# Kernel tuning notes

Measured on AMD Instinct MI355X. Metric: run time of the kernel, lower is better.

The kernel has to match this reference:

```python
import jax, jax.numpy as jnp
import numpy as np

B, CIN, COUT, H, W = 16, 128, 128, 64, 64
E, PS, FF = 8, 16, 8
GC, HID, HC = 4 * FF, 64, COUT * 4  # gate_channel, gate hidden, bottleneck hidden


def conv(x, w, stride=1, pad=0, groups=1):
    # x: [B,C,H,W], w: [O,I/groups,kh,kw]
    return jax.lax.conv_general_dilated(
        x, w, (stride, stride), [(pad, pad), (pad, pad)], feature_group_count=groups)


def group_norm(x, scale, bias, groups, eps=1e-5):
    b, c = x.shape[:2]
    xr = x.reshape(b, groups, c // groups, *x.shape[2:])
    m = xr.mean(axis=(2, 3, 4), keepdims=True)
    v = xr.var(axis=(2, 3, 4), keepdims=True)
    xr = (xr - m) * jax.lax.rsqrt(v + eps)
    return xr.reshape(x.shape) * scale[None, :, None, None] + bias[None, :, None, None]


def setup_inputs() -> dict:
    key = jax.random.key(0)
    ks = jax.random.split(key, 8)
    f = lambda k, shp: jax.random.normal(k, shp, jnp.float32) * 0.05
    return dict(
        x=jax.random.normal(ks[0], (B, CIN, H, W), jnp.float32),
        w_exp=f(ks[1], (E, COUT, CIN, 3, 3)),
        gn_exp_s=jnp.ones((E, COUT), jnp.float32),
        gn_exp_b=jnp.zeros((E, COUT), jnp.float32),
        w1=f(ks[2], (GC, HID)), b1=jnp.zeros((HID,), jnp.float32),
        w2=f(ks[3], (HID, E)), b2=jnp.zeros((E,), jnp.float32),
        w_pw1=f(ks[4], (HC, COUT, 1, 1)),
        gn1_s=jnp.ones((HC,), jnp.float32), gn1_b=jnp.zeros((HC,), jnp.float32),
        w_dw=f(ks[5], (HC, 1, 3, 3)),
        gn2_s=jnp.ones((HC,), jnp.float32), gn2_b=jnp.zeros((HC,), jnp.float32),
        w_pw2=f(ks[6], (COUT, HC, 1, 1)),
        gn3_s=jnp.ones((COUT,), jnp.float32), gn3_b=jnp.zeros((COUT,), jnp.float32),
    )


def reference(x, w_exp, gn_exp_s, gn_exp_b, w1, b1, w2, b2,
              w_pw1, gn1_s, gn1_b, w_dw, gn2_s, gn2_b, w_pw2, gn3_s, gn3_b):
    # ---- Conv experts (residual 3x3 conv + GN + SiLU), vmapped over experts ----
    def expert(w, s, b):
        y = conv(x, w, pad=1)
        y = group_norm(y, s, b, groups=min(8, COUT))
        return jax.nn.silu(y) + x  # use_residual=True, CIN == COUT

    ys = jax.vmap(expert)(w_exp, gn_exp_s, gn_exp_b)  # [E,B,C,H,W]

    # ---- Router gate: Fourier features of patch-center coordinates ----
    ph, pw = H // PS, W // PS
    cy = (jnp.arange(ph, dtype=jnp.float32) + 0.5) / ph
    cx = (jnp.arange(pw, dtype=jnp.float32) + 0.5) / pw
    freqs = (2.0 ** jnp.arange(FF, dtype=jnp.float32)) * jnp.pi
    ay = cy[:, None] * freqs  # [ph,FF]
    ax = cx[:, None] * freqs  # [pw,FF]
    feats = jnp.concatenate([
        jnp.broadcast_to(jnp.sin(ay)[:, None, :], (ph, pw, FF)),
        jnp.broadcast_to(jnp.cos(ay)[:, None, :], (ph, pw, FF)),
        jnp.broadcast_to(jnp.sin(ax)[None, :, :], (ph, pw, FF)),
        jnp.broadcast_to(jnp.cos(ax)[None, :, :], (ph, pw, FF)),
    ], axis=-1)  # [ph,pw,4*FF] == gate_channel
    hgate = jax.nn.silu(feats @ w1 + b1)
    wts = jax.nn.softmax(hgate @ w2 + b2, axis=-1)  # [ph,pw,E]

    # ---- Patch-wise combine of expert outputs ----
    wmap = jnp.repeat(jnp.repeat(wts, PS, axis=0), PS, axis=1)  # [H,W,E]
    combined = jnp.einsum('ebchw,hwe->bchw', ys, wmap)

    # ---- Inverted bottleneck: 1x1 -> dw3x3 -> 1x1(stride2) with GN+SiLU ----
    h = jax.nn.silu(group_norm(conv(combined, w_pw1), gn1_s, gn1_b, groups=8))
    h = jax.nn.silu(group_norm(conv(h, w_dw, pad=1, groups=HC), gn2_s, gn2_b, groups=8))
    h = jax.nn.silu(group_norm(conv(h, w_pw2, stride=2), gn3_s, gn3_b, groups=8))
    return h  # [B, COUT, H//2, W//2]
```

## Files before the change

kernel.cpp:

```cpp
#include <hip/hip_runtime.h>
#include <hip/hip_bf16.h>


#define B_ 16
#define CIN_ 128
#define COUT_ 128
#define H_ 64
#define W_ 64
#define HW_ 4096
#define E_ 8
#define FF_ 8
#define GC_ 32
#define HID_ 64
#define HC_ 512

typedef __hip_bfloat16 bf16;
typedef __bf16 bf16x8 __attribute__((ext_vector_type(8)));
typedef float f32x4 __attribute__((ext_vector_type(4)));
typedef float f32x16 __attribute__((ext_vector_type(16)));

__device__ __forceinline__ float siluf(float v) { return v / (1.f + __expf(-v)); }
__device__ __forceinline__ float bf2f(bf16 v) { return __bfloat162float(v); }
__device__ __forceinline__ bf16 f2bf(float v) { return __float2bfloat16(v); }

__device__ __forceinline__ void async16(void* lds, const void* g) {
  __builtin_amdgcn_global_load_lds(
      (const __attribute__((address_space(1))) unsigned int*)g,
      (__attribute__((address_space(3))) unsigned int*)lds, 16, 0, 0);
}

__global__ void gate_kernel(const float* __restrict__ w1, const float* __restrict__ b1,
                            const float* __restrict__ w2, const float* __restrict__ b2,
                            float* __restrict__ wts) {
  int p = threadIdx.x;
  if (p >= 16) return;
  int i = p >> 2, j = p & 3;
  float cy = (i + 0.5f) * 0.25f;
  float cx = (j + 0.5f) * 0.25f;
  float feats[GC_];
#pragma unroll
  for (int f = 0; f < FF_; ++f) {
    float fr = 3.14159265358979f * (float)(1 << f);
    float ay = cy * fr, ax = cx * fr;
    feats[f] = sinf(ay);
    feats[FF_ + f] = cosf(ay);
    feats[2 * FF_ + f] = sinf(ax);
    feats[3 * FF_ + f] = cosf(ax);
  }
  float hid[HID_];
  for (int k = 0; k < HID_; ++k) {
    float a = b1[k];
#pragma unroll
    for (int m = 0; m < GC_; ++m) a = fmaf(feats[m], w1[m * HID_ + k], a);
    hid[k] = siluf(a);
  }
  float lg[E_];
  float mx = -1e30f;
#pragma unroll
  for (int e = 0; e < E_; ++e) {
    float a = b2[e];
    for (int k = 0; k < HID_; ++k) a = fmaf(hid[k], w2[k * E_ + e], a);
    lg[e] = a;
    mx = fmaxf(mx, a);
  }
  float s = 0.f;
#pragma unroll
  for (int e = 0; e < E_; ++e) { lg[e] = __expf(lg[e] - mx); s += lg[e]; }
  float inv = 1.f / s;
#pragma unroll
  for (int e = 0; e < E_; ++e) wts[p * E_ + e] = lg[e] * inv;
}

__global__ __launch_bounds__(256) void xt_kernel(const float* __restrict__ x,
                                                 bf16* __restrict__ xT) {
  __shared__ float t[128][65];
  int b = blockIdx.x >> 6, h = blockIdx.x & 63;
  int tid = threadIdx.x;
  int w = tid & 63, c4 = tid >> 6;
  const float* xb = x + ((size_t)(b * 128) * 64 + h) * 64;
#pragma unroll 4
  for (int rep = 0; rep < 32; ++rep) {
    int ci = rep * 4 + c4;
    t[ci][w] = xb[(size_t)ci * HW_ + w];
  }
  __syncthreads();
  bf16* dst = xT + (size_t)(b * 64 + h) * 8192;
#pragma unroll 4
  for (int rep = 0; rep < 32; ++rep) {
    int o = rep * 256 + tid;
    int cg = o >> 9, w2 = (o >> 3) & 63, lo = o & 7;
    dst[o] = f2bf(t[cg * 8 + lo][w2]);
  }
}

__global__ void wt_kernel(const float* __restrict__ w_exp, bf16* __restrict__ wT) {
  int idx = blockIdx.x * 256 + threadIdx.x;
  if (idx >= 1179648) return;
  int lo = idx & 7;
  int co = (idx >> 3) & 127;
  int cg = (idx >> 10) & 15;
  int rest = idx >> 14;
  int tap = rest % 9, e = rest / 9;
  int ci = cg * 8 + lo;
  wT[idx] = f2bf(w_exp[(((size_t)(e * 128 + co) * 128 + ci) * 9) + tap]);
}

__global__ void wpT_kernel(const float* __restrict__ w_pw1, const float* __restrict__ w_pw2,
                           bf16* __restrict__ wp1T, bf16* __restrict__ wp2T) {
  int idx = blockIdx.x * 256 + threadIdx.x;
  if (idx < 65536) wp1T[idx] = f2bf(w_pw1[idx]);
  else if (idx < 131072) wp2T[idx - 65536] = f2bf(w_pw2[idx - 65536]);
}

__global__ __launch_bounds__(256, 2) void conv_mfma(
    const bf16* __restrict__ xT, const bf16* __restrict__ wT,
    float* __restrict__ statsE, bf16* __restrict__ ys) {
  __shared__ __align__(16) char xls[4 * 6336];
  __shared__ __align__(16) char wls[2][3 * 8192];
  __shared__ float red[4][8][2];

  int blk = blockIdx.x;
  int xcd = blk & 7;
  int r2 = blk >> 3;
  int b = xcd * 2 + (r2 & 1);
  int rest = r2 >> 1;
  int rt = rest & 15, e = rest >> 4;

  int tid = threadIdx.x, lane = tid & 63, wave = tid >> 6;
  int hi = lane >> 5, l31 = lane & 31;
  int h0 = rt * 4;

  if (tid < 48) {
    int cg = tid / 12, rem = tid % 12;
    int r = rem >> 1, edge = rem & 1;
    *(uint4*)(xls + cg * 6336 + r * 1056 + edge * 1040) = make_uint4(0u, 0u, 0u, 0u);
  }
  int rbad = (rt == 0) ? 0 : (rt == 15 ? 5 : -1);
  if (rbad >= 0) {
    int cg = tid >> 6, slot = (tid & 63) + 1;
    *(uint4*)(xls + cg * 6336 + rbad * 1056 + slot * 16) = make_uint4(0u, 0u, 0u, 0u);
  }

  f32x16 acc[4][2];
#pragma unroll
  for (int mt = 0; mt < 4; ++mt)
#pragma unroll
    for (int nt = 0; nt < 2; ++nt)
#pragma unroll
      for (int r = 0; r < 16; ++r) acc[mt][nt][r] = 0.f;

  for (int q = 0; q < 4; ++q) {
    if (q) __syncthreads();
    {
      int cg = wave;
#pragma unroll
      for (int r = 0; r < 6; ++r) {
        int h = h0 - 1 + r;
        if ((unsigned)h < 64u) {
          const char* g = (const char*)xT +
              ((size_t)((b * 64 + h) * 16) + q * 4 + cg) * 1024 + lane * 16;
          async16(xls + cg * 6336 + r * 1056 + 16, g);
        }
      }
    }
#pragma unroll
    for (int s = 0; s < 6; ++s) {
      int seg = wave * 6 + s;
      int tap = seg >> 3, rem = seg & 7;
      int cg = rem >> 1, cb = rem & 1;
      const char* g = (const char*)wT +
          ((size_t)(((e * 9 + tap) * 16) + q * 4 + cg) * 128 + cb * 64) * 16 + lane * 16;
      async16(wls[0] + (tap * 4 + cg) * 2048 + cb * 1024, g);
    }
    __syncthreads();

    for (int dr = 0; dr < 3; ++dr) {
      int buf = dr & 1;
      if (dr < 2) {
#pragma unroll
        for (int s = 0; s < 6; ++s) {
          int seg = wave * 6 + s;
          int tap = seg >> 3, rem = seg & 7;
          int cg = rem >> 1, cb = rem & 1;
          const char* g = (const char*)wT +
              ((size_t)(((e * 9 + (dr + 1) * 3 + tap) * 16) + q * 4 + cg) * 128 + cb * 64) * 16 +
              lane * 16;
          async16(wls[buf ^ 1] + (tap * 4 + cg) * 2048 + cb * 1024, g);
        }
      }
      int r_local = wave + dr;
      const char* wb = wls[buf];
      const char* xrow = xls;
      bf16x8 afp[2][2], bfp[2][2];
      {
        int cgl = hi;
        afp[0][0] = *(const bf16x8*)(wb + cgl * 2048 + (0 * 32 + l31) * 16);
        afp[0][1] = *(const bf16x8*)(wb + cgl * 2048 + (1 * 32 + l31) * 16);
        const char* xr = xrow + cgl * 6336 + r_local * 1056;
        bfp[0][0] = *(const bf16x8*)(xr + (0 * 32 + l31 + 0) * 16);
        bfp[0][1] = *(const bf16x8*)(xr + (1 * 32 + l31 + 0) * 16);
      }
#pragma unroll
      for (int s = 0; s < 12; ++s) {
        int mh = s & 1;
        int cura = s & 1, curb = (s >> 1) & 1;
        if (s < 11) {
          int s1 = s + 1;
          int ds1 = s1 >> 2, ks1 = (s1 >> 1) & 1, mh1 = s1 & 1;
          int cgl1 = ks1 * 2 + hi;
          const char* wt1 = wb + ds1 * 8192 + cgl1 * 2048;
          afp[s1 & 1][0] = *(const bf16x8*)(wt1 + ((mh1 * 2 + 0) * 32 + l31) * 16);
          afp[s1 & 1][1] = *(const bf16x8*)(wt1 + ((mh1 * 2 + 1) * 32 + l31) * 16);
          if (mh1 == 0) {
            const char* xr1 = xrow + cgl1 * 6336 + r_local * 1056;
            bfp[(s1 >> 1) & 1][0] = *(const bf16x8*)(xr1 + (0 * 32 + l31 + ds1) * 16);
            bfp[(s1 >> 1) & 1][1] = *(const bf16x8*)(xr1 + (1 * 32 + l31 + ds1) * 16);
          }
        }
#pragma unroll
        for (int i = 0; i < 2; ++i)
#pragma unroll
          for (int nt = 0; nt < 2; ++nt)
            acc[mh * 2 + i][nt] = __builtin_amdgcn_mfma_f32_32x32x16_bf16(
                afp[cura][i], bfp[curb][nt], acc[mh * 2 + i][nt], 0, 0, 0);
      }
      if (dr < 2) __syncthreads();
    }
  }

  int hh = h0 + wave;
  bf16* yb = ys + (size_t)((e * 16 + b) * 128) * 4096;
#pragma unroll
  for (int mt = 0; mt < 4; ++mt) {
    float s0 = 0.f, ss0 = 0.f, s1 = 0.f, ss1 = 0.f;
#pragma unroll
    for (int nt = 0; nt < 2; ++nt) {
      int w = nt * 32 + l31;
      int pos = hh * 64 + w;
#pragma unroll
      for (int r = 0; r < 16; ++r) {
        float v = acc[mt][nt][r];
        if (r < 8) { s0 += v; ss0 += v * v; } else { s1 += v; ss1 += v * v; }
        int row = (r & 3) + 8 * (r >> 2) + 4 * hi;
        yb[(size_t)(mt * 32 + row) * 4096 + pos] = f2bf(v);
      }
    }
#pragma unroll
    for (int off = 32; off; off >>= 1) {
      s0 += __shfl_down(s0, off, 64);
      ss0 += __shfl_down(ss0, off, 64);
      s1 += __shfl_down(s1, off, 64);
      ss1 += __shfl_down(ss1, off, 64);
    }
    if (lane == 0) {
      red[wave][mt * 2][0] = s0; red[wave][mt * 2][1] = ss0;
      red[wave][mt * 2 + 1][0] = s1; red[wave][mt * 2 + 1][1] = ss1;
    }
  }
  __syncthreads();
  if (tid < 16) {
    int g = tid >> 1, which = tid & 1;
    float t = red[0][g][which] + red[1][g][which] + red[2][g][which] + red[3][g][which];
    atomicAdd(&statsE[((e * 16 + b) * 8 + g) * 2 + which], t);
  }
}

__global__ void finalize_stats(float* __restrict__ st, int n, float inv) {
  int i = blockIdx.x * 256 + threadIdx.x;
  if (i >= n) return;
  float S = st[i * 2], SS = st[i * 2 + 1];
  float mean = S * inv;
  float var = SS * inv - mean * mean;
  st[i * 2] = mean;
  st[i * 2 + 1] = rsqrtf(var + 1e-5f);
}

__global__ __launch_bounds__(256) void combine_cl(
    const float* __restrict__ x, const bf16* __restrict__ ys,
    const float* __restrict__ st, const float* __restrict__ gns,
    const float* __restrict__ gnb, const float* __restrict__ wts,
    bf16* __restrict__ ccl) {
  __shared__ bf16 tile[64][132];
  int b = blockIdx.x >> 6, h = blockIdx.x & 63;
  int t = threadIdx.x;
  int w32 = t & 31, coq = t >> 5;
  float m_[8], r_[8];
#pragma unroll
  for (int e = 0; e < 8; ++e) {
    m_[e] = st[((e * 16 + b) * 8 + coq) * 2];
    r_[e] = st[((e * 16 + b) * 8 + coq) * 2 + 1];
  }
#pragma unroll
  for (int wt2 = 0; wt2 < 2; ++wt2) {
    int w = wt2 * 32 + w32;
    int pid = (h >> 4) * 4 + (w >> 4);
    int pos = h * 64 + w;
    float wt_[8];
#pragma unroll
    for (int e = 0; e < 8; ++e) wt_[e] = wts[pid * 8 + e];
    for (int coi = 0; coi < 16; ++coi) {
      int co = coq * 16 + coi;
      float v = x[((size_t)(b * 128 + co) << 12) + pos];
#pragma unroll
      for (int e = 0; e < 8; ++e) {
        float y = bf2f(ys[((size_t)((e * 16 + b) * 128 + co) << 12) + pos]);
        float yn = (y - m_[e]) * r_[e] * gns[e * 128 + co] + gnb[e * 128 + co];
        v += siluf(yn) * wt_[e];
      }
      tile[w][co] = f2bf(v);
    }
  }
  __syncthreads();
  int row = t >> 2, q = t & 3;
  char* dst = (char*)ccl + ((size_t)(b * 4096 + h * 64 + row)) * 256 + q * 64;
  const char* src = (const char*)&tile[row][0] + q * 64;
#pragma unroll
  for (int i = 0; i < 4; ++i)
    *(uint4*)(dst + i * 16) = *(const uint4*)(src + i * 16);
}

__global__ __launch_bounds__(256) void pw1_mfma(
    const bf16* __restrict__ ccl, const bf16* __restrict__ wp1T,
    bf16* __restrict__ h1cl, float* __restrict__ stats1) {
  __shared__ __align__(16) char ls[65536];
  __shared__ float red[4][2][2];
  char* als = ls;
  char* bls = ls + 32768;
  int blk = blockIdx.x;
  int ntile = blk & 511, mtile = blk >> 9;
  int n0 = ntile * 128, m0 = mtile * 128;
  int t = threadIdx.x, lane = t & 63, wave = t >> 6;
  int quad = lane >> 4, l15 = lane & 15;
  int b = n0 >> 12;

#pragma unroll
  for (int i = 0; i < 8; ++i) {
    int id = t + 256 * i;
    int r = id >> 4, c = id & 15;
    *(uint4*)(als + c * 2048 + r * 16) =
        *(const uint4*)((const char*)wp1T + (size_t)(m0 + r) * 256 + c * 16);
    *(uint4*)(bls + c * 2048 + r * 16) =
        *(const uint4*)((const char*)ccl + (size_t)(n0 + r) * 256 + c * 16);
  }
  __syncthreads();

  f32x4 acc[8][2];
#pragma unroll
  for (int mt = 0; mt < 8; ++mt)
#pragma unroll
    for (int nt = 0; nt < 2; ++nt) acc[mt][nt] = (f32x4){0.f, 0.f, 0.f, 0.f};

#pragma unroll
  for (int kc = 0; kc < 4; ++kc) {
    int cgq = kc * 4 + quad;
    bf16x8 af[8];
#pragma unroll
    for (int mt = 0; mt < 8; ++mt)
      af[mt] = *(const bf16x8*)(als + cgq * 2048 + (mt * 16 + l15) * 16);
    bf16x8 bfr[2];
#pragma unroll
    for (int nt = 0; nt < 2; ++nt)
      bfr[nt] = *(const bf16x8*)(bls + cgq * 2048 + (wave * 32 + nt * 16 + l15) * 16);
#pragma unroll
    for (int mt = 0; mt < 8; ++mt)
#pragma unroll
      for (int nt = 0; nt < 2; ++nt)
        acc[mt][nt] = __builtin_amdgcn_mfma_f32_16x16x32_bf16(
            af[mt], bfr[nt], acc[mt][nt], 0, 0, 0);
  }

  __syncthreads();
  float s[2] = {0.f, 0.f}, ss[2] = {0.f, 0.f};
  bf16* tile = (bf16*)ls;
#pragma unroll
  for (int mt = 0; mt < 8; ++mt) {
    int gi = mt >> 2;
#pragma unroll
    for (int nt = 0; nt < 2; ++nt) {
      int n = wave * 32 + nt * 16 + l15;
#pragma unroll
      for (int r = 0; r < 4; ++r) {
        float v = acc[mt][nt][r];
        s[gi] += v;
        ss[gi] += v * v;
        tile[n * 132 + mt * 16 + quad * 4 + r] = f2bf(v);
      }
    }
  }
#pragma unroll
  for (int gi = 0; gi < 2; ++gi) {
#pragma unroll
    for (int off = 32; off; off >>= 1) {
      s[gi] += __shfl_down(s[gi], off, 64);
      ss[gi] += __shfl_down(ss[gi], off, 64);
    }
  }
  if (lane == 0) {
    red[wave][0][0] = s[0]; red[wave][0][1] = ss[0];
    red[wave][1][0] = s[1]; red[wave][1][1] = ss[1];
  }
  __syncthreads();
  if (t < 4) {
    int gi = t >> 1, which = t & 1;
    float v = red[0][gi][which] + red[1][gi][which] + red[2][gi][which] + red[3][gi][which];
    atomicAdd(&stats1[(b * 8 + mtile * 2 + gi) * 2 + which], v);
  }
#pragma unroll
  for (int i = 0; i < 8; ++i) {
    int id = t + 256 * i;
    int r = id >> 4, q = id & 15;
    char* dst = (char*)h1cl + (size_t)(n0 + r) * 1024 + m0 * 2 + q * 16;
    const char* src = (const char*)tile + r * 264 + q * 16;
    *(uint4*)dst = *(const uint4*)src;
  }
}

__global__ __launch_bounds__(256) void dw_cl(
    const bf16* __restrict__ h1cl, const float* __restrict__ w_dw,
    const float* __restrict__ st1, const float* __restrict__ gs,
    const float* __restrict__ gb, bf16* __restrict__ h2cl,
    float* __restrict__ stats2) {
  __shared__ __align__(16) bf16 tile[18 * 66 * 16];
  __shared__ float red2[4][2];
  int blk = blockIdx.x;
  int ht = blk & 3, hcg = (blk >> 2) & 31, b = blk >> 7;
  int h0 = ht * 16;
  int hc0 = hcg * 16;
  int hcb = hcg >> 2;
  int t = threadIdx.x;

  float mean = st1[(b * 8 + hcb) * 2], rstd = st1[(b * 8 + hcb) * 2 + 1];
  float scale[16], shift[16];
#pragma unroll
  for (int j = 0; j < 16; ++j) {
    float g = gs[hc0 + j];
    scale[j] = rstd * g;
    shift[j] = gb[hc0 + j] - mean * rstd * g;
  }

  for (int i = 0; i < 5; ++i) {
    int idx = t + 256 * i;
    if (idx >= 1188) break;
    int row = idx / 66, wslot = idx - row * 66;
    int hh = h0 - 1 + row;
    int w = wslot - 1;
    int swz = (wslot >> 2) & 3;
    bf16* dst = tile + (row * 66 + wslot) * 16;
    if ((unsigned)hh < 64u && (unsigned)w < 64u) {
      const char* p = (const char*)h1cl + ((size_t)(b * 4096 + hh * 64 + w) * 512 + hc0) * 2;
      uint4 a0 = *(const uint4*)p;
      uint4 a1 = *(const uint4*)(p + 16);
      const bf16* pv = (const bf16*)&a0;
      const bf16* pv1 = (const bf16*)&a1;
      bf16 outv[16];
#pragma unroll
      for (int j = 0; j < 8; ++j)
        outv[j] = f2bf(siluf(bf2f(pv[j]) * scale[j] + shift[j]));
#pragma unroll
      for (int j = 0; j < 8; ++j)
        outv[8 + j] = f2bf(siluf(bf2f(pv1[j]) * scale[8 + j] + shift[8 + j]));
#pragma unroll
      for (int qq = 0; qq < 4; ++qq) {
        int ph = (qq + swz) & 3;
        *(uint2*)(dst + ph * 4) = *(const uint2*)(outv + qq * 4);
      }
    } else {
      *(uint4*)dst = make_uint4(0u, 0u, 0u, 0u);
      *(uint4*)(dst + 8) = make_uint4(0u, 0u, 0u, 0u);
    }
  }
  __syncthreads();

  int w = t & 63, q = t >> 6;
  float wv[9][4];
#pragma unroll
  for (int j = 0; j < 4; ++j) {
    int hc = hc0 + q * 4 + j;
#pragma unroll
    for (int tap = 0; tap < 9; ++tap) wv[tap][j] = w_dw[hc * 9 + tap];
  }

  f32x4 win[3][3];
  float acc_s = 0.f, acc_ss = 0.f;

  auto ld4 = [&](int r, int dwi) -> f32x4 {
    int slot = w + dwi;
    int ph = (q + (slot >> 2)) & 3;
    const bf16* p = tile + (r * 66 + slot) * 16 + ph * 4;
    uint2 u = *(const uint2*)p;
    const bf16* pb = (const bf16*)&u;
    return (f32x4){bf2f(pb[0]), bf2f(pb[1]), bf2f(pb[2]), bf2f(pb[3])};
  };

#pragma unroll
  for (int dwi = 0; dwi < 3; ++dwi) {
    win[0][dwi] = ld4(0, dwi);
    win[1][dwi] = ld4(1, dwi);
  }
#pragma unroll
  for (int orow = 0; orow < 16; ++orow) {
    int rnew = orow + 2;
    int ringn = rnew % 3;
#pragma unroll
    for (int dwi = 0; dwi < 3; ++dwi) win[ringn][dwi] = ld4(rnew, dwi);
    f32x4 acc = (f32x4){0.f, 0.f, 0.f, 0.f};
#pragma unroll
    for (int dr = 0; dr < 3; ++dr) {
      int ring = (orow + dr) % 3;
#pragma unroll
      for (int dwi = 0; dwi < 3; ++dwi) {
#pragma unroll
        for (int j = 0; j < 4; ++j)
          acc[j] = fmaf(win[ring][dwi][j], wv[dr * 3 + dwi][j], acc[j]);
      }
    }
#pragma unroll
    for (int j = 0; j < 4; ++j) { acc_s += acc[j]; acc_ss += acc[j] * acc[j]; }
    if (!(orow & 1) && !(w & 1)) {
      int hglob = h0 + orow;
      int pos2 = (hglob >> 1) * 32 + (w >> 1);
      bf16 tmp[4];
#pragma unroll
      for (int j = 0; j < 4; ++j) tmp[j] = f2bf(acc[j]);
      *(uint2*)((char*)h2cl + ((size_t)(b * 1024 + pos2) * 512 + hc0 + q * 4) * 2) =
          *(const uint2*)tmp;
    }
  }

#pragma unroll
  for (int off = 32; off; off >>= 1) {
    acc_s += __shfl_down(acc_s, off, 64);
    acc_ss += __shfl_down(acc_ss, off, 64);
  }
  int wave = t >> 6;
  if ((t & 63) == 0) { red2[wave][0] = acc_s; red2[wave][1] = acc_ss; }
  __syncthreads();
  if (t < 2) {
    float v = red2[0][t] + red2[1][t] + red2[2][t] + red2[3][t];
    atomicAdd(&stats2[(b * 8 + hcb) * 2 + t], v);
  }
}

__global__ void norm2_kernel(bf16* __restrict__ h2, const float* __restrict__ st2,
                             const float* __restrict__ gs, const float* __restrict__ gb) {
  int tg = blockIdx.x * 256 + threadIdx.x;
  int e8 = tg * 8;
  int hc0 = e8 & 511;
  int rest = e8 >> 9;
  int bq = rest >> 10;
  int g = hc0 >> 6;
  float mean = st2[(bq * 8 + g) * 2], rstd = st2[(bq * 8 + g) * 2 + 1];
  uint4 v = *(const uint4*)((const char*)h2 + (size_t)tg * 16);
  bf16* pv = (bf16*)&v;
  bf16 outv[8];
#pragma unroll
  for (int j = 0; j < 8; ++j) {
    float x = bf2f(pv[j]);
    x = (x - mean) * rstd * gs[hc0 + j] + gb[hc0 + j];
    outv[j] = f2bf(siluf(x));
  }
  *(uint4*)((char*)h2 + (size_t)tg * 16) = *(const uint4*)outv;
}

__global__ __launch_bounds__(256) void pw2_mfma(
    const bf16* __restrict__ h2n, const bf16* __restrict__ wp2T,
    float* __restrict__ h3, float* __restrict__ stats3) {
  __shared__ __align__(16) char als[2][8192];
  __shared__ __align__(16) char bls[2][4096];
  __shared__ float red[4][8][2];
  int blk = blockIdx.x;
  int n0 = blk * 64;
  int b = n0 >> 10, posb = n0 & 1023;
  int t = threadIdx.x, lane = t & 63, wave = t >> 6;
  int quad = lane >> 4, l15 = lane & 15;
  int wbase = wave * 16;

  f32x4 acc[8];
#pragma unroll
  for (int mt = 0; mt < 8; ++mt) acc[mt] = (f32x4){0.f, 0.f, 0.f, 0.f};

  {
#pragma unroll
    for (int i = 0; i < 2; ++i) {
      int id = t + 256 * i;
      int c4 = id >> 7, r = id & 127;
      *(uint4*)(als[0] + c4 * 2048 + r * 16) =
          *(const uint4*)((const char*)wp2T + (size_t)r * 1024 + c4 * 16);
    }
    int c4 = t >> 6, r = t & 63;
    *(uint4*)(bls[0] + c4 * 1024 + r * 16) =
        *(const uint4*)((const char*)h2n + (size_t)(n0 + r) * 1024 + c4 * 16);
  }
  for (int kc = 0; kc < 16; ++kc) {
    __syncthreads();
    if (kc + 1 < 16) {
      int nb = (kc + 1) & 1;
#pragma unroll
      for (int i = 0; i < 2; ++i) {
        int id = t + 256 * i;
        int c4 = id >> 7, r = id & 127;
        *(uint4*)(als[nb] + c4 * 2048 + r * 16) =
            *(const uint4*)((const char*)wp2T + (size_t)r * 1024 + ((kc + 1) * 4 + c4) * 16);
      }
      int c4 = t >> 6, r = t & 63;
      *(uint4*)(bls[nb] + c4 * 1024 + r * 16) =
          *(const uint4*)((const char*)h2n + (size_t)(n0 + r) * 1024 + ((kc + 1) * 4 + c4) * 16);
    }
    int buf = kc & 1;
    bf16x8 bf1 = *(const bf16x8*)(bls[buf] + quad * 1024 + (wbase + l15) * 16);
#pragma unroll
    for (int mt = 0; mt < 8; ++mt) {
      bf16x8 af = *(const bf16x8*)(als[buf] + quad * 2048 + (mt * 16 + l15) * 16);
      acc[mt] = __builtin_amdgcn_mfma_f32_16x16x32_bf16(af, bf1, acc[mt], 0, 0, 0);
    }
  }

#pragma unroll
  for (int mt = 0; mt < 8; ++mt) {
    float s = 0.f, ss = 0.f;
    int pos = posb + wbase + l15;
#pragma unroll
    for (int r = 0; r < 4; ++r) {
      float v = acc[mt][r];
      s += v;
      ss += v * v;
      int co = mt * 16 + quad * 4 + r;
      h3[(size_t)(b * 128 + co) * 1024 + pos] = v;
    }
#pragma unroll
    for (int off = 32; off; off >>= 1) {
      s += __shfl_down(s, off, 64);
      ss += __shfl_down(ss, off, 64);
    }
    if (lane == 0) { red[wave][mt][0] = s; red[wave][mt][1] = ss; }
  }
  __syncthreads();
  if (t < 16) {
    int mt = t >> 1, which = t & 1;
    float v = red[0][mt][which] + red[1][mt][which] + red[2][mt][which] + red[3][mt][which];
    atomicAdd(&stats3[(b * 8 + mt) * 2 + which], v);
  }
}

__global__ void out_kernel(const float* __restrict__ h3, const float* __restrict__ stats,
                           const float* __restrict__ gs, const float* __restrict__ gb,
                           float* __restrict__ out) {
  const int total = B_ * COUT_ * 1024;
  for (int idx = blockIdx.x * blockDim.x + threadIdx.x; idx < total; idx += gridDim.x * blockDim.x) {
    int c = (idx >> 10) & 127;
    int b = idx >> 17;
    int bg = b * 8 + (c >> 4);
    float S = stats[bg * 2], SS = stats[bg * 2 + 1];
    float mean = S * (1.f / 16384.f);
    float var = SS * (1.f / 16384.f) - mean * mean;
    float rstd = rsqrtf(var + 1e-5f);
    float v = (h3[idx] - mean) * rstd * gs[c] + gb[c];
    out[idx] = siluf(v);
  }
}

extern "C" void kernel_launch(void* const* d_in, const int* in_sizes, int n_in,
                              void* d_out, int out_size, void* d_ws, size_t ws_size,
                              hipStream_t stream) {
  const float* x = (const float*)d_in[0];
  const float* w_exp = (const float*)d_in[1];
  const float* gn_exp_s = (const float*)d_in[2];
  const float* gn_exp_b = (const float*)d_in[3];
  const float* w1 = (const float*)d_in[4];
  const float* b1 = (const float*)d_in[5];
  const float* w2 = (const float*)d_in[6];
  const float* b2 = (const float*)d_in[7];
  const float* w_pw1 = (const float*)d_in[8];
  const float* gn1_s = (const float*)d_in[9];
  const float* gn1_b = (const float*)d_in[10];
  const float* w_dw = (const float*)d_in[11];
  const float* gn2_s = (const float*)d_in[12];
  const float* gn2_b = (const float*)d_in[13];
  const float* w_pw2 = (const float*)d_in[14];
  const float* gn3_s = (const float*)d_in[15];
  const float* gn3_b = (const float*)d_in[16];

  char* ws = (char*)d_ws;
  const size_t WP1T_OFF = 16384;
  const size_t WP2T_OFF = WP1T_OFF + 131072;
  const size_t XT_OFF = WP2T_OFF + 131072;
  const size_t WT_OFF = XT_OFF + 16777216;
  const size_t YS_OFF = WT_OFF + 2359296;
  const size_t NEEDED = YS_OFF + 134217728;
  if (ws_size < NEEDED) return;

  float* wts = (float*)ws;
  float* stats1 = (float*)(ws + 1024);
  float* stats2 = (float*)(ws + 2048);
  float* stats3 = (float*)(ws + 3072);
  float* statsE = (float*)(ws + 4096);
  bf16* wp1T = (bf16*)(ws + WP1T_OFF);
  bf16* wp2T = (bf16*)(ws + WP2T_OFF);
  bf16* xT = (bf16*)(ws + XT_OFF);
  bf16* ccl = (bf16*)(ws + XT_OFF);
  bf16* wT = (bf16*)(ws + WT_OFF);
  bf16* ys = (bf16*)(ws + YS_OFF);
  bf16* h1cl = (bf16*)(ws + YS_OFF);
  bf16* h2cl = (bf16*)(ws + YS_OFF + 67108864);
  float* h3 = (float*)(ws + YS_OFF + 83886080);

  hipMemsetAsync(ws, 0, 16384, stream);
  gate_kernel<<<1, 64, 0, stream>>>(w1, b1, w2, b2, wts);
  xt_kernel<<<B_ * 64, 256, 0, stream>>>(x, xT);
  wt_kernel<<<4608, 256, 0, stream>>>(w_exp, wT);
  wpT_kernel<<<512, 256, 0, stream>>>(w_pw1, w_pw2, wp1T, wp2T);
  conv_mfma<<<E_ * B_ * 16, 256, 0, stream>>>(xT, wT, statsE, ys);
  finalize_stats<<<4, 256, 0, stream>>>(statsE, 1024, 1.f / 65536.f);
  combine_cl<<<B_ * 64, 256, 0, stream>>>(x, ys, statsE, gn_exp_s, gn_exp_b, wts, ccl);
  pw1_mfma<<<4 * 512, 256, 0, stream>>>(ccl, wp1T, h1cl, stats1);
  finalize_stats<<<1, 128, 0, stream>>>(stats1, 128, 1.f / 262144.f);
  dw_cl<<<B_ * 32 * 4, 256, 0, stream>>>(h1cl, w_dw, stats1, gn1_s, gn1_b, h2cl, stats2);
  finalize_stats<<<1, 128, 0, stream>>>(stats2, 128, 1.f / 262144.f);
  norm2_kernel<<<4096, 256, 0, stream>>>(h2cl, stats2, gn2_s, gn2_b);
  pw2_mfma<<<256, 256, 0, stream>>>(h2cl, wp2T, h3, stats3);
  out_kernel<<<1024, 256, 0, stream>>>(h3, stats3, gn3_s, gn3_b, (float*)d_out);
}
```

Baseline: 484.1 us.

## Fold stats finalization into consumers, fuse GN2 into pw2 load, vectorize combine

Removes the three finalize_stats launches; each consumer kernel now computes mean and rstd from the raw sums itself. The separate norm2 pass over h2 is folded into pw2_mfma's B-tile load, which removes one full read and write of the 32 MB intermediate. combine_cl is restructured so each thread handles 8 contiguous pixels with vector loads of x and ys and a precomputed scale and shift. The cost is redundant per-thread stats math and GN/SiLU work inside the GEMM load path.

```diff
diff --git a/kernel.cpp b/kernel.cpp
--- a/kernel.cpp
+++ b/kernel.cpp
@@ -265,50 +265,55 @@
   }
 }
 
-__global__ void finalize_stats(float* __restrict__ st, int n, float inv) {
-  int i = blockIdx.x * 256 + threadIdx.x;
-  if (i >= n) return;
-  float S = st[i * 2], SS = st[i * 2 + 1];
-  float mean = S * inv;
-  float var = SS * inv - mean * mean;
-  st[i * 2] = mean;
-  st[i * 2 + 1] = rsqrtf(var + 1e-5f);
-}
-
 __global__ __launch_bounds__(256) void combine_cl(
     const float* __restrict__ x, const bf16* __restrict__ ys,
-    const float* __restrict__ st, const float* __restrict__ gns,
+    const float* __restrict__ stE, const float* __restrict__ gns,
     const float* __restrict__ gnb, const float* __restrict__ wts,
     bf16* __restrict__ ccl) {
   __shared__ bf16 tile[64][132];
   int b = blockIdx.x >> 6, h = blockIdx.x & 63;
   int t = threadIdx.x;
-  int w32 = t & 31, coq = t >> 5;
-  float m_[8], r_[8];
+  int oct = t & 7, cq = t >> 3;
+  int w0 = oct * 8;
+  int gidx = cq >> 2;
+  int pid = (h >> 4) * 4 + (w0 >> 4);
+  int pos = h * 64 + w0;
+
+  float m_[8], r_[8], wt_[8];
 #pragma unroll
   for (int e = 0; e < 8; ++e) {
-    m_[e] = st[((e * 16 + b) * 8 + coq) * 2];
-    r_[e] = st[((e * 16 + b) * 8 + coq) * 2 + 1];
-  }
-#pragma unroll
-  for (int wt2 = 0; wt2 < 2; ++wt2) {
-    int w = wt2 * 32 + w32;
-    int pid = (h >> 4) * 4 + (w >> 4);
-    int pos = h * 64 + w;
-    float wt_[8];
-#pragma unroll
-    for (int e = 0; e < 8; ++e) wt_[e] = wts[pid * 8 + e];
-    for (int coi = 0; coi < 16; ++coi) {
-      int co = coq * 16 + coi;
-      float v = x[((size_t)(b * 128 + co) << 12) + pos];
-#pragma unroll
-      for (int e = 0; e < 8; ++e) {
-        float y = bf2f(ys[((size_t)((e * 16 + b) * 128 + co) << 12) + pos]);
-        float yn = (y - m_[e]) * r_[e] * gns[e * 128 + co] + gnb[e * 128 + co];
-        v += siluf(yn) * wt_[e];
-      }
-      tile[w][co] = f2bf(v);
-    }
+    float S = stE[((e * 16 + b) * 8 + gidx) * 2];
+    float SS = stE[((e * 16 + b) * 8 + gidx) * 2 + 1];
+    float mean = S * (1.f / 65536.f);
+    float var = SS * (1.f / 65536.f) - mean * mean;
+    m_[e] = mean;
+    r_[e] = rsqrtf(var + 1e-5f);
+    wt_[e] = wts[pid * 8 + e];
+  }
+
+#pragma unroll
+  for (int k = 0; k < 4; ++k) {
+    int co = cq * 4 + k;
+    const float* xp = x + ((size_t)(b * 128 + co) << 12) + pos;
+    float v[8];
+    float4 xa = *(const float4*)xp;
+    float4 xb2 = *(const float4*)(xp + 4);
+    v[0] = xa.x; v[1] = xa.y; v[2] = xa.z; v[3] = xa.w;
+    v[4] = xb2.x; v[5] = xb2.y; v[6] = xb2.z; v[7] = xb2.w;
+#pragma unroll
+    for (int e = 0; e < 8; ++e) {
+      uint4 u = *(const uint4*)(ys + ((size_t)((e * 16 + b) * 128 + co) << 12) + pos);
+      const bf16* pv = (const bf16*)&u;
+      float sc = r_[e] * gns[e * 128 + co];
+      float sh = gnb[e * 128 + co] - m_[e] * sc;
+#pragma unroll
+      for (int j = 0; j < 8; ++j) {
+        float yn = bf2f(pv[j]) * sc + sh;
+        v[j] = fmaf(siluf(yn), wt_[e], v[j]);
+      }
+    }
+#pragma unroll
+    for (int j = 0; j < 8; ++j) tile[w0 + j][co] = f2bf(v[j]);
   }
   __syncthreads();
   int row = t >> 2, q = t & 3;
@@ -429,7 +434,10 @@
   int hcb = hcg >> 2;
   int t = threadIdx.x;
 
-  float mean = st1[(b * 8 + hcb) * 2], rstd = st1[(b * 8 + hcb) * 2 + 1];
+  float S1 = st1[(b * 8 + hcb) * 2], SS1 = st1[(b * 8 + hcb) * 2 + 1];
+  float mean = S1 * (1.f / 262144.f);
+  float var1 = SS1 * (1.f / 262144.f) - mean * mean;
+  float rstd = rsqrtf(var1 + 1e-5f);
   float scale[16], shift[16];
 #pragma unroll
   for (int j = 0; j < 16; ++j) {
@@ -541,30 +549,11 @@
   }
 }
 
-__global__ void norm2_kernel(bf16* __restrict__ h2, const float* __restrict__ st2,
-                             const float* __restrict__ gs, const float* __restrict__ gb) {
-  int tg = blockIdx.x * 256 + threadIdx.x;
-  int e8 = tg * 8;
-  int hc0 = e8 & 511;
-  int rest = e8 >> 9;
-  int bq = rest >> 10;
-  int g = hc0 >> 6;
-  float mean = st2[(bq * 8 + g) * 2], rstd = st2[(bq * 8 + g) * 2 + 1];
-  uint4 v = *(const uint4*)((const char*)h2 + (size_t)tg * 16);
-  bf16* pv = (bf16*)&v;
-  bf16 outv[8];
-#pragma unroll
-  for (int j = 0; j < 8; ++j) {
-    float x = bf2f(pv[j]);
-    x = (x - mean) * rstd * gs[hc0 + j] + gb[hc0 + j];
-    outv[j] = f2bf(siluf(x));
-  }
-  *(uint4*)((char*)h2 + (size_t)tg * 16) = *(const uint4*)outv;
-}
-
 __global__ __launch_bounds__(256) void pw2_mfma(
-    const bf16* __restrict__ h2n, const bf16* __restrict__ wp2T,
-    float* __restrict__ h3, float* __restrict__ stats3) {
+    const bf16* __restrict__ h2, const bf16* __restrict__ wp2T,
+    const float* __restrict__ st2, const float* __restrict__ gs2,
+    const float* __restrict__ gb2, float* __restrict__ h3,
+    float* __restrict__ stats3) {
   __shared__ __align__(16) char als[2][8192];
   __shared__ __align__(16) char bls[2][4096];
   __shared__ float red[4][8][2];
@@ -574,6 +563,26 @@
   int t = threadIdx.x, lane = t & 63, wave = t >> 6;
   int quad = lane >> 4, l15 = lane & 15;
   int wbase = wave * 16;
+  int c4 = t >> 6, r = t & 63;
+
+  auto load_bls = [&](char* dst, int kc) {
+    int hc0 = (kc * 4 + c4) * 8;
+    int g = hc0 >> 6;
+    float S = st2[(b * 8 + g) * 2], SS = st2[(b * 8 + g) * 2 + 1];
+    float mean = S * (1.f / 262144.f);
+    float rstd = rsqrtf(SS * (1.f / 262144.f) - mean * mean + 1e-5f);
+    uint4 u = *(const uint4*)((const char*)h2 + (size_t)(n0 + r) * 1024 +
+                              (size_t)(kc * 4 + c4) * 16);
+    const bf16* pv = (const bf16*)&u;
+    bf16 outv[8];
+#pragma unroll
+    for (int j = 0; j < 8; ++j) {
+      float xv = bf2f(pv[j]);
+      xv = (xv - mean) * rstd * gs2[hc0 + j] + gb2[hc0 + j];
+      outv[j] = f2bf(siluf(xv));
+    }
+    *(uint4*)dst = *(const uint4*)outv;
+  };
 
   f32x4 acc[8];
 #pragma unroll
@@ -583,14 +592,13 @@
 #pragma unroll
     for (int i = 0; i < 2; ++i) {
       int id = t + 256 * i;
-      int c4 = id >> 7, r = id & 127;
-      *(uint4*)(als[0] + c4 * 2048 + r * 16) =
-          *(const uint4*)((const char*)wp2T + (size_t)r * 1024 + c4 * 16);
-    }
-    int c4 = t >> 6, r = t & 63;
-    *(uint4*)(bls[0] + c4 * 1024 + r * 16) =
-        *(const uint4*)((const char*)h2n + (size_t)(n0 + r) * 1024 + c4 * 16);
-  }
+      int cc = id >> 7, rr = id & 127;
+      *(uint4*)(als[0] + cc * 2048 + rr * 16) =
+          *(const uint4*)((const char*)wp2T + (size_t)rr * 1024 + cc * 16);
+    }
+    load_bls(bls[0] + c4 * 1024 + r * 16, 0);
+  }
+#pragma unroll
   for (int kc = 0; kc < 16; ++kc) {
     __syncthreads();
     if (kc + 1 < 16) {
@@ -598,13 +606,11 @@
 #pragma unroll
       for (int i = 0; i < 2; ++i) {
         int id = t + 256 * i;
-        int c4 = id >> 7, r = id & 127;
-        *(uint4*)(als[nb] + c4 * 2048 + r * 16) =
-            *(const uint4*)((const char*)wp2T + (size_t)r * 1024 + ((kc + 1) * 4 + c4) * 16);
-      }
-      int c4 = t >> 6, r = t & 63;
-      *(uint4*)(bls[nb] + c4 * 1024 + r * 16) =
-          *(const uint4*)((const char*)h2n + (size_t)(n0 + r) * 1024 + ((kc + 1) * 4 + c4) * 16);
+        int cc = id >> 7, rr = id & 127;
+        *(uint4*)(als[nb] + cc * 2048 + rr * 16) =
+            *(const uint4*)((const char*)wp2T + (size_t)rr * 1024 + ((kc + 1) * 4 + cc) * 16);
+      }
+      load_bls(bls[nb] + c4 * 1024 + r * 16, kc + 1);
     }
     int buf = kc & 1;
     bf16x8 bf1 = *(const bf16x8*)(bls[buf] + quad * 1024 + (wbase + l15) * 16);
@@ -620,11 +626,11 @@
     float s = 0.f, ss = 0.f;
     int pos = posb + wbase + l15;
 #pragma unroll
-    for (int r = 0; r < 4; ++r) {
-      float v = acc[mt][r];
+    for (int rr = 0; rr < 4; ++rr) {
+      float v = acc[mt][rr];
       s += v;
       ss += v * v;
-      int co = mt * 16 + quad * 4 + r;
+      int co = mt * 16 + quad * 4 + rr;
       h3[(size_t)(b * 128 + co) * 1024 + pos] = v;
     }
 #pragma unroll
@@ -710,13 +716,9 @@
   wt_kernel<<<4608, 256, 0, stream>>>(w_exp, wT);
   wpT_kernel<<<512, 256, 0, stream>>>(w_pw1, w_pw2, wp1T, wp2T);
   conv_mfma<<<E_ * B_ * 16, 256, 0, stream>>>(xT, wT, statsE, ys);
-  finalize_stats<<<4, 256, 0, stream>>>(statsE, 1024, 1.f / 65536.f);
   combine_cl<<<B_ * 64, 256, 0, stream>>>(x, ys, statsE, gn_exp_s, gn_exp_b, wts, ccl);
   pw1_mfma<<<4 * 512, 256, 0, stream>>>(ccl, wp1T, h1cl, stats1);
-  finalize_stats<<<1, 128, 0, stream>>>(stats1, 128, 1.f / 262144.f);
   dw_cl<<<B_ * 32 * 4, 256, 0, stream>>>(h1cl, w_dw, stats1, gn1_s, gn1_b, h2cl, stats2);
-  finalize_stats<<<1, 128, 0, stream>>>(stats2, 128, 1.f / 262144.f);
-  norm2_kernel<<<4096, 256, 0, stream>>>(h2cl, stats2, gn2_s, gn2_b);
-  pw2_mfma<<<256, 256, 0, stream>>>(h2cl, wp2T, h3, stats3);
+  pw2_mfma<<<256, 256, 0, stream>>>(h2cl, wp2T, stats2, gn2_s, gn2_b, h3, stats3);
   out_kernel<<<1024, 256, 0, stream>>>(h3, stats3, gn3_s, gn3_b, (float*)d_out);
 }
```

Result: no change. 481.7 us (-0.5%).
